# Kernel optimization log

Hardware: AMD Instinct MI355X
Metric: run time of the kernel (lower is better)

Reference implementation:

```python
import jax, jax.numpy as jnp
import numpy as np

EPS = 1e-06  # slot-attention renorm epsilon
LN_EPS = 1e-05  # torch LayerNorm default
NUM_ITERS = 3


def layernorm(x, w, b):
    m = jnp.mean(x, axis=-1, keepdims=True)
    v = jnp.mean((x - m) ** 2, axis=-1, keepdims=True)
    return (x - m) * jax.lax.rsqrt(v + LN_EPS) * w + b


def setup_inputs() -> dict:
    key = jax.random.key(0)
    ks = jax.random.split(key, 16)
    B, N, D = 32, 4096, 512
    S, NS, H = 128, 8, 256
    def lin(k, out_f, in_f):
        return jax.random.normal(k, (out_f, in_f), jnp.float32) * (1.0 / np.sqrt(in_f))
    return {
        "inputs": jax.random.normal(ks[0], (B, N, D), jnp.float32),
        "slots_init": jax.random.normal(ks[1], (B, NS, S), jnp.float32),
        "ln_in_w": jnp.ones((D,), jnp.float32), "ln_in_b": jnp.zeros((D,), jnp.float32),
        "ln_slot_w": jnp.ones((S,), jnp.float32), "ln_slot_b": jnp.zeros((S,), jnp.float32),
        "ln_mlp_w": jnp.ones((S,), jnp.float32), "ln_mlp_b": jnp.zeros((S,), jnp.float32),
        "Wq": lin(ks[2], S, S), "Wk": lin(ks[3], S, D), "Wv": lin(ks[4], S, D),
        "gru_Wih": lin(ks[5], 3 * S, S), "gru_Whh": lin(ks[6], 3 * S, S),
        "gru_bih": jnp.zeros((3 * S,), jnp.float32), "gru_bhh": jnp.zeros((3 * S,), jnp.float32),
        "mlp_W1": lin(ks[7], H, S), "mlp_b1": jnp.zeros((H,), jnp.float32),
        "mlp_W2": lin(ks[8], S, H), "mlp_b2": jnp.zeros((S,), jnp.float32),
        "slots_mu": jax.random.normal(ks[9], (1, 1, S), jnp.float32) * 0.1,
        "slots_log_sigma": jax.random.normal(ks[10], (1, 1, S), jnp.float32) * 0.1,
    }


def gru_cell(x, h, Wih, Whh, bih, bhh):
    # PyTorch GRUCell math. x, h: [BS, S]
    S = h.shape[-1]
    gi = x @ Wih.T + bih
    gh = h @ Whh.T + bhh
    i_r, i_z, i_n = gi[:, :S], gi[:, S:2 * S], gi[:, 2 * S:]
    h_r, h_z, h_n = gh[:, :S], gh[:, S:2 * S], gh[:, 2 * S:]
    r = jax.nn.sigmoid(i_r + h_r)
    z = jax.nn.sigmoid(i_z + h_z)
    n = jnp.tanh(i_n + r * h_n)
    return (1.0 - z) * n + z * h


def reference(inputs, slots_init, ln_in_w, ln_in_b, ln_slot_w, ln_slot_b, ln_mlp_w, ln_mlp_b,
              Wq, Wk, Wv, gru_Wih, gru_Whh, gru_bih, gru_bhh,
              mlp_W1, mlp_b1, mlp_W2, mlp_b2, slots_mu, slots_log_sigma):
    B, N, D = inputs.shape
    NS, S = slots_init.shape[1], slots_init.shape[2]
    x = layernorm(inputs, ln_in_w, ln_in_b)
    k = jnp.einsum('bnd,sd->bns', x, Wk)  # [B,N,S]
    v = jnp.einsum('bnd,sd->bns', x, Wv)
    slots = slots_mu + jnp.exp(slots_log_sigma) * slots_init  # [B,NS,S]
    scale = S ** (-0.5)
    for _ in range(NUM_ITERS):
        slots_prev = slots
        q = jnp.einsum('bmd,sd->bms', layernorm(slots, ln_slot_w, ln_slot_b), Wq)  # [B,NS,S]
        attn_logits = scale * jnp.einsum('bns,bms->bnm', k, q)  # [B,N,NS]
        attn = jax.nn.softmax(attn_logits, axis=-1) + EPS
        attn = attn / jnp.sum(attn, axis=1, keepdims=True)  # normalize over inputs
        updates = jnp.einsum('bnm,bns->bms', attn, v)  # [B,NS,S]
        h = gru_cell(updates.reshape(B * NS, S), slots_prev.reshape(B * NS, S),
                     gru_Wih, gru_Whh, gru_bih, gru_bhh).reshape(B, NS, S)
        mlp_out = jnp.maximum(layernorm(h, ln_mlp_w, ln_mlp_b) @ mlp_W1.T + mlp_b1, 0.0) @ mlp_W2.T + mlp_b2
        slots = h + mlp_out
    return slots
```

## Files before the change

### kernel.cpp

```cpp
#include <hip/hip_runtime.h>

typedef __bf16 v8bf __attribute__((ext_vector_type(8)));
typedef __bf16 v4bf __attribute__((ext_vector_type(4)));
typedef float  v4f  __attribute__((ext_vector_type(4)));
typedef unsigned short u16;

#define LN_EPS_F 1e-5f
#define ATTN_EPS 1e-6f

static constexpr int Bsz = 32;
static constexpr int Nn  = 4096;
static constexpr int Dd  = 512;
static constexpr int Ss  = 128;
static constexpr int NSs = 8;
static constexpr int Hh  = 256;
static constexpr int MROWS = Bsz * Nn;

__device__ __forceinline__ void load_lds16(const void* g, void* l) {
    __builtin_amdgcn_global_load_lds(
        (const __attribute__((address_space(1))) void*)g,
        (__attribute__((address_space(3))) void*)l, 16, 0, 0);
}

__global__ __launch_bounds__(256) void k_cast(const float* __restrict__ X,
                                              u16* __restrict__ Xb,
                                              float2* __restrict__ stats) {
    const int wid = threadIdx.x >> 6, lane = threadIdx.x & 63;
    const int row = blockIdx.x * 4 + wid;
    const float4* xp = reinterpret_cast<const float4*>(X + (size_t)row * Dd) + lane * 2;
    float4 a = xp[0];
    float4 b = xp[1];
    float s  = a.x + a.y + a.z + a.w + b.x + b.y + b.z + b.w;
    float s2 = a.x*a.x + a.y*a.y + a.z*a.z + a.w*a.w
             + b.x*b.x + b.y*b.y + b.z*b.z + b.w*b.w;
    v8bf o;
    o[0] = (__bf16)a.x; o[1] = (__bf16)a.y; o[2] = (__bf16)a.z; o[3] = (__bf16)a.w;
    o[4] = (__bf16)b.x; o[5] = (__bf16)b.y; o[6] = (__bf16)b.z; o[7] = (__bf16)b.w;
    *reinterpret_cast<v8bf*>(Xb + (size_t)row * Dd + lane * 8) = o;
#pragma unroll
    for (int off = 32; off > 0; off >>= 1) {
        s  += __shfl_xor(s, off);
        s2 += __shfl_xor(s2, off);
    }
    if (lane == 0) {
        float m = s * (1.0f / Dd);
        float v = s2 * (1.0f / Dd) - m * m;
        stats[row] = make_float2(m, rsqrtf(v + LN_EPS_F));
    }
}

__global__ __launch_bounds__(256) void k_prep(const float* __restrict__ Wk, const float* __restrict__ Wv,
                                              const float* __restrict__ ln_in_w, const float* __restrict__ ln_in_b,
                                              const float* __restrict__ slots_init, const float* __restrict__ mu,
                                              const float* __restrict__ lsig,
                                              u16* __restrict__ Wkvp, float* __restrict__ cb,
                                              float* __restrict__ Scol, float* __restrict__ slots) {
    const int bid = blockIdx.x;
    const int t = threadIdx.x;
    if (bid < 512) {
        int idx = bid * 256 + t;
        int n = idx >> 9, d = idx & 511;
        float w = (n < Ss) ? Wk[n * Dd + d] : Wv[(n - Ss) * Dd + d];
        w *= ln_in_w[d];
        __bf16 bv = (__bf16)w;
        Wkvp[idx] = __builtin_bit_cast(u16, bv);
    } else if (bid < 640) {
        int idx = (bid - 512) * 256 + t;
        int sidx = idx & (Ss - 1);
        slots[idx] = mu[sidx] + expf(lsig[sidx]) * slots_init[idx];
    } else {
        const int wid = t >> 6, lane = t & 63;
        const int rowbase = (bid - 640) * 32 + wid * 8;
        const int d0 = lane * 8;
        float4 lw0 = *reinterpret_cast<const float4*>(ln_in_w + d0);
        float4 lw1 = *reinterpret_cast<const float4*>(ln_in_w + d0 + 4);
        float4 lb0 = *reinterpret_cast<const float4*>(ln_in_b + d0);
        float4 lb1 = *reinterpret_cast<const float4*>(ln_in_b + d0 + 4);
        for (int rr = 0; rr < 8; ++rr) {
            int row = rowbase + rr;
            const float* wrow = (row < Ss) ? (Wk + (size_t)row * Dd)
                                           : (Wv + (size_t)(row - Ss) * Dd);
            float4 w0 = *reinterpret_cast<const float4*>(wrow + d0);
            float4 w1 = *reinterpret_cast<const float4*>(wrow + d0 + 4);
            float accb = lb0.x*w0.x + lb0.y*w0.y + lb0.z*w0.z + lb0.w*w0.w
                       + lb1.x*w1.x + lb1.y*w1.y + lb1.z*w1.z + lb1.w*w1.w;
            float accs = (float)(__bf16)(w0.x*lw0.x) + (float)(__bf16)(w0.y*lw0.y)
                       + (float)(__bf16)(w0.z*lw0.z) + (float)(__bf16)(w0.w*lw0.w)
                       + (float)(__bf16)(w1.x*lw1.x) + (float)(__bf16)(w1.y*lw1.y)
                       + (float)(__bf16)(w1.z*lw1.z) + (float)(__bf16)(w1.w*lw1.w);
#pragma unroll
            for (int off = 32; off > 0; off >>= 1) {
                accb += __shfl_xor(accb, off);
                accs += __shfl_xor(accs, off);
            }
            if (lane == 0) { cb[row] = accb; Scol[row] = accs; }
        }
    }
}

__global__ __launch_bounds__(512, 2) void k_kvgemm(const u16* __restrict__ Xb,
                                                   const float2* __restrict__ stats,
                                                   const u16* __restrict__ Wkvp,
                                                   const float* __restrict__ cb,
                                                   const float* __restrict__ Scol,
                                                   u16* __restrict__ kv) {
    __shared__ __bf16 As[2][256 * 64];
    __shared__ __bf16 Bsh[2][256 * 64];
    __shared__ float2 stats_sh[256];
    const int t    = threadIdx.x;
    const int lane = t & 63;
    const int w    = t >> 6;
    const int wr   = w >> 2;
    const int wc   = w & 3;
    const int lr   = lane & 15;
    const int g    = lane >> 4;
    const int r7   = lane & 7;
    const size_t m0 = (size_t)blockIdx.x * 256;

    const int rowoff = lane >> 3;
    const int swz8   = ((lane & 7) ^ rowoff) * 8;
    const u16* asrc = Xb   + (m0 + w * 32 + rowoff) * 512 + swz8;
    const u16* bsrc = Wkvp + (size_t)(w * 32 + rowoff) * 512 + swz8;

    if (t < 256) stats_sh[t] = stats[m0 + t];

    const v4f vzero = {0.f, 0.f, 0.f, 0.f};
    v4f acc[8][4];
#pragma unroll
    for (int i = 0; i < 8; ++i)
#pragma unroll
        for (int j = 0; j < 4; ++j) acc[i][j] = vzero;

#define STAGE(buf, kb)                                                          \
    {                                                                           \
        _Pragma("unroll")                                                       \
        for (int i = 0; i < 4; ++i) {                                           \
            load_lds16(asrc + (size_t)i * 8 * 512 + (kb) * 64,                  \
                       &As[buf][(w * 32 + i * 8) * 64]);                        \
            load_lds16(bsrc + (size_t)i * 8 * 512 + (kb) * 64,                  \
                       &Bsh[buf][(w * 32 + i * 8) * 64]);                       \
        }                                                                       \
    }

    STAGE(0, 0);
    asm volatile("s_waitcnt vmcnt(0) lgkmcnt(0)" ::: "memory");
    __builtin_amdgcn_s_barrier();

    int buf = 0;
#pragma unroll
    for (int kb = 0; kb < 8; ++kb) {
        if (kb < 7) STAGE(buf ^ 1, kb + 1);
#pragma unroll
        for (int ks = 0; ks < 2; ++ks) {
            const int co = ((ks * 4 + g) ^ r7) * 8;
            v8bf a[8], b[4];
#pragma unroll
            for (int mi = 0; mi < 8; ++mi)
                a[mi] = *reinterpret_cast<const v8bf*>(
                    &As[buf][(wr * 128 + mi * 16 + lr) * 64 + co]);
#pragma unroll
            for (int ni = 0; ni < 4; ++ni)
                b[ni] = *reinterpret_cast<const v8bf*>(
                    &Bsh[buf][(wc * 64 + ni * 16 + lr) * 64 + co]);
#pragma unroll
            for (int ni = 0; ni < 4; ++ni)
#pragma unroll
                for (int mi = 0; mi < 8; ++mi)
                    acc[mi][ni] = __builtin_amdgcn_mfma_f32_16x16x32_bf16(a[mi], b[ni], acc[mi][ni], 0, 0, 0);
        }
        asm volatile("s_waitcnt vmcnt(0)" ::: "memory");
        __builtin_amdgcn_s_barrier();
        buf ^= 1;
    }
#undef STAGE
    float Sn[4], cbv[4];
#pragma unroll
    for (int ni = 0; ni < 4; ++ni) {
        int col = wc * 64 + ni * 16 + lr;
        Sn[ni]  = Scol[col];
        cbv[ni] = cb[col];
    }
#pragma unroll
    for (int mi = 0; mi < 8; ++mi)
#pragma unroll
        for (int j = 0; j < 4; ++j) {
            int rl = wr * 128 + mi * 16 + g * 4 + j;
            float2 st = stats_sh[rl];
            size_t mg = m0 + rl;
#pragma unroll
            for (int ni = 0; ni < 4; ++ni) {
                int col = wc * 64 + ni * 16 + lr;
                float val = st.y * (acc[mi][ni][j] - st.x * Sn[ni]) + cbv[ni];
                __bf16 bv = (__bf16)val;
                kv[mg * 256 + col] = __builtin_bit_cast(u16, bv);
            }
        }
}

__global__ __launch_bounds__(128) void k_q(const float* __restrict__ slots,
                                           const float* __restrict__ lnw, const float* __restrict__ lnb,
                                           const float* __restrict__ Wq, float* __restrict__ q) {
    __shared__ float xs[128];
    __shared__ float red[4];
    const int t = threadIdx.x;
    const int bm = blockIdx.x;
    float x = slots[bm * 128 + t];
    float s = x, s2 = x * x;
#pragma unroll
    for (int off = 32; off > 0; off >>= 1) { s += __shfl_xor(s, off); s2 += __shfl_xor(s2, off); }
    const int wid = t >> 6, lane = t & 63;
    if (lane == 0) { red[wid * 2] = s; red[wid * 2 + 1] = s2; }
    __syncthreads();
    float S1 = red[0] + red[2], S2 = red[1] + red[3];
    float m = S1 * (1.f / 128.f);
    float rstd = rsqrtf(S2 * (1.f / 128.f) - m * m + LN_EPS_F);
    xs[t] = (x - m) * rstd * lnw[t] + lnb[t];
    __syncthreads();
    const float* wr = Wq + (size_t)t * 128;
    float acc = 0.f;
#pragma unroll 8
    for (int d = 0; d < 128; d += 4) {
        float4 w = *reinterpret_cast<const float4*>(wr + d);
        acc += w.x * xs[d] + w.y * xs[d + 1] + w.z * xs[d + 2] + w.w * xs[d + 3];
    }
    q[bm * 128 + t] = acc * 0.08838834764831845f;
}

__global__ __launch_bounds__(256) void k_attnupd(const u16* __restrict__ kv, const float* __restrict__ q,
                                                 float* __restrict__ upd_part, float* __restrict__ colsum_part) {
    __shared__ float qs[8 * 128];
    __shared__ float at[128][8];
    __shared__ __bf16 vt[128][128];
    __shared__ float colpart[4][8];
    const int b  = blockIdx.y;
    const int ch = blockIdx.x;
    const int t  = threadIdx.x;
    const int lane = t & 63, wv = t >> 6;
    *reinterpret_cast<float4*>(&qs[t * 4]) = *reinterpret_cast<const float4*>(&q[b * 1024 + t * 4]);
    __syncthreads();
    {
        const int rsub = lane >> 4;
        const int csub = (lane & 15) * 8;
#pragma unroll
        for (int p = 0; p < 8; ++p) {
            int row = wv * 32 + p * 4;
            const u16* src = kv + ((size_t)(b * Nn + ch * 128 + row + rsub)) * 256 + 128 + csub;
            load_lds16(src, &vt[row][0]);
        }
    }
    const int nl   = t >> 1;
    const int half = t & 1;
    const u16* krow = kv + ((size_t)(b * Nn + ch * 128 + nl)) * 256 + half * 64;
    float acc[8] = {0.f, 0.f, 0.f, 0.f, 0.f, 0.f, 0.f, 0.f};
#pragma unroll
    for (int c = 0; c < 8; ++c) {
        v8bf kvv = *reinterpret_cast<const v8bf*>(krow + c * 8);
        float kf[8];
#pragma unroll
        for (int j = 0; j < 8; ++j) kf[j] = (float)kvv[j];
#pragma unroll
        for (int m = 0; m < 8; ++m) {
            const float* qrow = &qs[m * 128 + half * 64 + c * 8];
            float aa = 0.f;
#pragma unroll
            for (int j = 0; j < 8; ++j) aa += kf[j] * qrow[j];
            acc[m] += aa;
        }
    }
#pragma unroll
    for (int m = 0; m < 8; ++m) acc[m] += __shfl_xor(acc[m], 1);
    float mx = acc[0];
#pragma unroll
    for (int m = 1; m < 8; ++m) mx = fmaxf(mx, acc[m]);
    float e[8]; float ssum = 0.f;
#pragma unroll
    for (int m = 0; m < 8; ++m) { e[m] = __expf(acc[m] - mx); ssum += e[m]; }
    float inv = 1.0f / ssum;
    float a8[8];
#pragma unroll
    for (int m = 0; m < 8; ++m) a8[m] = e[m] * inv + ATTN_EPS;
    *reinterpret_cast<float4*>(&at[nl][half * 4]) =
        make_float4(a8[half * 4], a8[half * 4 + 1], a8[half * 4 + 2], a8[half * 4 + 3]);
#pragma unroll
    for (int m = 0; m < 8; ++m) {
        float v = a8[m];
#pragma unroll
        for (int off = 32; off > 0; off >>= 1) v += __shfl_xor(v, off);
        if (lane == 0) colpart[wv][m] = v * 0.5f;
    }
    __syncthreads();
    const int m2 = t >> 5;
    const int s0 = (t & 31) * 4;
    float a0 = 0.f, a1 = 0.f, a2 = 0.f, a3 = 0.f;
#pragma unroll 4
    for (int n = 0; n < 128; ++n) {
        float a = at[n][m2];
        v4bf vvv = *reinterpret_cast<const v4bf*>(&vt[n][s0]);
        a0 += a * (float)vvv[0];
        a1 += a * (float)vvv[1];
        a2 += a * (float)vvv[2];
        a3 += a * (float)vvv[3];
    }
    *reinterpret_cast<float4*>(upd_part + ((size_t)(b * 32 + ch) * 8 + m2) * 128 + s0) =
        make_float4(a0, a1, a2, a3);
    if (t < 8)
        colsum_part[(b * 32 + ch) * 8 + t] =
            colpart[0][t] + colpart[1][t] + colpart[2][t] + colpart[3][t];
}

__global__ __launch_bounds__(256) void k_finishq(const float* __restrict__ upd_part,
                                                 const float* __restrict__ colsum_part,
                                                 const float* __restrict__ slots_in,
                                                 const float* __restrict__ Wih, const float* __restrict__ Whh,
                                                 const float* __restrict__ bih, const float* __restrict__ bhh,
                                                 const float* __restrict__ lnw, const float* __restrict__ lnb,
                                                 const float* __restrict__ W1, const float* __restrict__ b1,
                                                 const float* __restrict__ W2, const float* __restrict__ b2,
                                                 const float* __restrict__ lnsw, const float* __restrict__ lnsb,
                                                 const float* __restrict__ Wq,
                                                 float* __restrict__ slots_out, float* __restrict__ qout) {
    __shared__ float us[128], sp[128], hnorm[128], qsrc[128], act[256];
    __shared__ float upart[2][128];
    __shared__ float gpart[2][6][128];
    __shared__ float p2[2][128];
    __shared__ float qpart[2][128];
    __shared__ float red[4];
    __shared__ float csum_sh;
    const int t   = threadIdx.x;
    const int tid = t & 127, half = t >> 7;
    const int bm  = blockIdx.x;
    const int b = bm >> 3, m = bm & 7;
    if (t < 64) {
        float v = (t < 32) ? colsum_part[(b * 32 + t) * 8 + m] : 0.f;
#pragma unroll
        for (int off = 32; off > 0; off >>= 1) v += __shfl_xor(v, off);
        if (t == 0) csum_sh = v;
    }
    float u = 0.f;
#pragma unroll 4
    for (int chk = half * 16; chk < half * 16 + 16; ++chk)
        u += upd_part[((size_t)(b * 32 + chk) * 8 + m) * 128 + tid];
    upart[half][tid] = u;
    if (half == 0) sp[tid] = slots_in[bm * 128 + tid];
    __syncthreads();
    if (half == 0) us[tid] = (upart[0][tid] + upart[1][tid]) * (1.f / csum_sh);
    __syncthreads();
    {
        const int d0g = half * 64;
        float a_r = 0.f, a_z = 0.f, a_n = 0.f, b_r = 0.f, b_z = 0.f, b_n = 0.f;
        const float* Wr = Wih + (size_t)tid * 128 + d0g;
        const float* Wz = Wih + (size_t)(128 + tid) * 128 + d0g;
        const float* Wn = Wih + (size_t)(256 + tid) * 128 + d0g;
        const float* Vr = Whh + (size_t)tid * 128 + d0g;
        const float* Vz = Whh + (size_t)(128 + tid) * 128 + d0g;
        const float* Vn = Whh + (size_t)(256 + tid) * 128 + d0g;
#pragma unroll 4
        for (int d = 0; d < 64; d += 4) {
            float u0 = us[d0g + d], u1 = us[d0g + d + 1], u2 = us[d0g + d + 2], u3 = us[d0g + d + 3];
            float p0 = sp[d0g + d], p1 = sp[d0g + d + 1], p2_ = sp[d0g + d + 2], p3 = sp[d0g + d + 3];
            float4 w;
            w = *reinterpret_cast<const float4*>(Wr + d); a_r += w.x*u0 + w.y*u1 + w.z*u2 + w.w*u3;
            w = *reinterpret_cast<const float4*>(Wz + d); a_z += w.x*u0 + w.y*u1 + w.z*u2 + w.w*u3;
            w = *reinterpret_cast<const float4*>(Wn + d); a_n += w.x*u0 + w.y*u1 + w.z*u2 + w.w*u3;
            w = *reinterpret_cast<const float4*>(Vr + d); b_r += w.x*p0 + w.y*p1 + w.z*p2_ + w.w*p3;
            w = *reinterpret_cast<const float4*>(Vz + d); b_z += w.x*p0 + w.y*p1 + w.z*p2_ + w.w*p3;
            w = *reinterpret_cast<const float4*>(Vn + d); b_n += w.x*p0 + w.y*p1 + w.z*p2_ + w.w*p3;
        }
        gpart[half][0][tid] = a_r; gpart[half][1][tid] = a_z; gpart[half][2][tid] = a_n;
        gpart[half][3][tid] = b_r; gpart[half][4][tid] = b_z; gpart[half][5][tid] = b_n;
    }
    __syncthreads();
    float gir = bih[tid]       + gpart[0][0][tid] + gpart[1][0][tid];
    float giz = bih[128 + tid] + gpart[0][1][tid] + gpart[1][1][tid];
    float gin = bih[256 + tid] + gpart[0][2][tid] + gpart[1][2][tid];
    float ghr = bhh[tid]       + gpart[0][3][tid] + gpart[1][3][tid];
    float ghz = bhh[128 + tid] + gpart[0][4][tid] + gpart[1][4][tid];
    float ghn = bhh[256 + tid] + gpart[0][5][tid] + gpart[1][5][tid];
    float h0 = sp[tid];
    float r  = 1.f / (1.f + __expf(-(gir + ghr)));
    float z  = 1.f / (1.f + __expf(-(giz + ghz)));
    float nn = tanhf(gin + r * ghn);
    float h  = (1.f - z) * nn + z * h0;
    if (half == 0) {
        float s = h, s2 = h * h;
#pragma unroll
        for (int off = 32; off > 0; off >>= 1) { s += __shfl_xor(s, off); s2 += __shfl_xor(s2, off); }
        if ((t & 63) == 0) { red[(tid >> 6) * 2] = s; red[(tid >> 6) * 2 + 1] = s2; }
    }
    __syncthreads();
    {
        float S1 = red[0] + red[2], S2 = red[1] + red[3];
        float mean = S1 * (1.f / Ss);
        float rstd = rsqrtf(S2 * (1.f / Ss) - mean * mean + LN_EPS_F);
        if (half == 0) hnorm[tid] = (h - mean) * rstd * lnw[tid] + lnb[tid];
    }
    __syncthreads();
    {
        float a = b1[t];
        const float* w1r = W1 + (size_t)t * 128;
#pragma unroll 4
        for (int d = 0; d < 128; d += 4) {
            float4 w = *reinterpret_cast<const float4*>(w1r + d);
            a += w.x * hnorm[d] + w.y * hnorm[d + 1] + w.z * hnorm[d + 2] + w.w * hnorm[d + 3];
        }
        act[t] = fmaxf(a, 0.f);
    }
    __syncthreads();
    {
        float o = 0.f;
        const int j0 = half * 128;
        const float* w2r = W2 + (size_t)tid * 256 + j0;
#pragma unroll 4
        for (int j = 0; j < 128; j += 4) {
            float4 w = *reinterpret_cast<const float4*>(w2r + j);
            o += w.x * act[j0 + j] + w.y * act[j0 + j + 1] + w.z * act[j0 + j + 2] + w.w * act[j0 + j + 3];
        }
        p2[half][tid] = o;
    }
    __syncthreads();
    float snew = h + b2[tid] + p2[0][tid] + p2[1][tid];
    if (half == 0) slots_out[bm * 128 + tid] = snew;
    if (half == 0) {
        float s = snew, s2 = snew * snew;
#pragma unroll
        for (int off = 32; off > 0; off >>= 1) { s += __shfl_xor(s, off); s2 += __shfl_xor(s2, off); }
        if ((t & 63) == 0) { red[(tid >> 6) * 2] = s; red[(tid >> 6) * 2 + 1] = s2; }
    }
    __syncthreads();
    {
        float T1 = red[0] + red[2], T2 = red[1] + red[3];
        float m2 = T1 * (1.f / Ss);
        float rstd2 = rsqrtf(T2 * (1.f / Ss) - m2 * m2 + LN_EPS_F);
        if (half == 0) qsrc[tid] = (snew - m2) * rstd2 * lnsw[tid] + lnsb[tid];
    }
    __syncthreads();
    {
        float qa = 0.f;
        const int d0g = half * 64;
        const float* wr = Wq + (size_t)tid * 128 + d0g;
#pragma unroll 4
        for (int d = 0; d < 64; d += 4) {
            float4 w = *reinterpret_cast<const float4*>(wr + d);
            qa += w.x * qsrc[d0g + d] + w.y * qsrc[d0g + d + 1] + w.z * qsrc[d0g + d + 2] + w.w * qsrc[d0g + d + 3];
        }
        qpart[half][tid] = qa;
    }
    __syncthreads();
    if (half == 0)
        qout[bm * 128 + tid] = (qpart[0][tid] + qpart[1][tid]) * 0.08838834764831845f;
}

extern "C" void kernel_launch(void* const* d_in, const int* in_sizes, int n_in,
                              void* d_out, int out_size, void* d_ws, size_t ws_size,
                              hipStream_t stream) {
    const float* X          = (const float*)d_in[0];
    const float* slots_init = (const float*)d_in[1];
    const float* ln_in_w    = (const float*)d_in[2];
    const float* ln_in_b    = (const float*)d_in[3];
    const float* ln_slot_w  = (const float*)d_in[4];
    const float* ln_slot_b  = (const float*)d_in[5];
    const float* ln_mlp_w   = (const float*)d_in[6];
    const float* ln_mlp_b   = (const float*)d_in[7];
    const float* Wq         = (const float*)d_in[8];
    const float* Wk         = (const float*)d_in[9];
    const float* Wv         = (const float*)d_in[10];
    const float* gWih       = (const float*)d_in[11];
    const float* gWhh       = (const float*)d_in[12];
    const float* gbih       = (const float*)d_in[13];
    const float* gbhh       = (const float*)d_in[14];
    const float* W1         = (const float*)d_in[15];
    const float* b1         = (const float*)d_in[16];
    const float* W2         = (const float*)d_in[17];
    const float* b2         = (const float*)d_in[18];
    const float* mu         = (const float*)d_in[19];
    const float* lsig       = (const float*)d_in[20];

    char* p = (char*)d_ws;
    u16*    Wkvp        = (u16*)p;    p += (size_t)256 * 512 * sizeof(u16);
    float*  cb          = (float*)p;  p += 256 * sizeof(float);
    float*  Scol        = (float*)p;  p += 256 * sizeof(float);
    float*  slots       = (float*)p;  p += 32 * 8 * 128 * sizeof(float);
    float*  qbuf        = (float*)p;  p += 32 * 8 * 128 * sizeof(float);
    float*  colsum_part = (float*)p;  p += 32 * 32 * 8 * sizeof(float);
    float*  upd_part    = (float*)p;  p += (size_t)32 * 32 * 8 * 128 * sizeof(float);
    u16*    kv          = (u16*)p;    p += (size_t)MROWS * 256 * sizeof(u16);
    u16*    Xb          = (u16*)p;    p += (size_t)MROWS * Dd * sizeof(u16);
    float2* stats       = (float2*)p; p += (size_t)MROWS * sizeof(float2);

    k_cast<<<MROWS / 4, 256, 0, stream>>>(X, Xb, stats);
    k_prep<<<648, 256, 0, stream>>>(Wk, Wv, ln_in_w, ln_in_b, slots_init, mu, lsig,
                                    Wkvp, cb, Scol, slots);
    k_kvgemm<<<MROWS / 256, 512, 0, stream>>>(Xb, stats, Wkvp, cb, Scol, kv);
    k_q<<<256, 128, 0, stream>>>(slots, ln_slot_w, ln_slot_b, Wq, qbuf);

    for (int it = 0; it < 3; ++it) {
        k_attnupd<<<dim3(32, 32), 256, 0, stream>>>(kv, qbuf, upd_part, colsum_part);
        k_finishq<<<256, 256, 0, stream>>>(upd_part, colsum_part, slots,
                                           gWih, gWhh, gbih, gbhh,
                                           ln_mlp_w, ln_mlp_b, W1, b1, W2, b2,
                                           ln_slot_w, ln_slot_b, Wq,
                                           (it == 2) ? (float*)d_out : slots, qbuf);
    }
}
```

Baseline: 317.6 us.

## Fold Wk/Wv projections into slot side, attend directly over normalized inputs

```diff
diff --git a/kernel.cpp b/kernel.cpp
--- a/kernel.cpp
+++ b/kernel.cpp
@@ -49,152 +49,37 @@
     }
 }
 
-__global__ __launch_bounds__(256) void k_prep(const float* __restrict__ Wk, const float* __restrict__ Wv,
-                                              const float* __restrict__ ln_in_w, const float* __restrict__ ln_in_b,
-                                              const float* __restrict__ slots_init, const float* __restrict__ mu,
+__global__ __launch_bounds__(256) void k_prep(const float* __restrict__ Wv,
+                                              const float* __restrict__ ln_in_b,
+                                              const float* __restrict__ slots_init,
+                                              const float* __restrict__ mu,
                                               const float* __restrict__ lsig,
-                                              u16* __restrict__ Wkvp, float* __restrict__ cb,
-                                              float* __restrict__ Scol, float* __restrict__ slots) {
+                                              float* __restrict__ cbv0,
+                                              float* __restrict__ slots) {
     const int bid = blockIdx.x;
     const int t = threadIdx.x;
-    if (bid < 512) {
+    if (bid < 128) {
         int idx = bid * 256 + t;
-        int n = idx >> 9, d = idx & 511;
-        float w = (n < Ss) ? Wk[n * Dd + d] : Wv[(n - Ss) * Dd + d];
-        w *= ln_in_w[d];
-        __bf16 bv = (__bf16)w;
-        Wkvp[idx] = __builtin_bit_cast(u16, bv);
-    } else if (bid < 640) {
-        int idx = (bid - 512) * 256 + t;
         int sidx = idx & (Ss - 1);
         slots[idx] = mu[sidx] + expf(lsig[sidx]) * slots_init[idx];
     } else {
         const int wid = t >> 6, lane = t & 63;
-        const int rowbase = (bid - 640) * 32 + wid * 8;
+        const int rowbase = (bid - 128) * 32 + wid * 8;
         const int d0 = lane * 8;
-        float4 lw0 = *reinterpret_cast<const float4*>(ln_in_w + d0);
-        float4 lw1 = *reinterpret_cast<const float4*>(ln_in_w + d0 + 4);
         float4 lb0 = *reinterpret_cast<const float4*>(ln_in_b + d0);
         float4 lb1 = *reinterpret_cast<const float4*>(ln_in_b + d0 + 4);
         for (int rr = 0; rr < 8; ++rr) {
             int row = rowbase + rr;
-            const float* wrow = (row < Ss) ? (Wk + (size_t)row * Dd)
-                                           : (Wv + (size_t)(row - Ss) * Dd);
+            const float* wrow = Wv + (size_t)row * Dd;
             float4 w0 = *reinterpret_cast<const float4*>(wrow + d0);
             float4 w1 = *reinterpret_cast<const float4*>(wrow + d0 + 4);
             float accb = lb0.x*w0.x + lb0.y*w0.y + lb0.z*w0.z + lb0.w*w0.w
                        + lb1.x*w1.x + lb1.y*w1.y + lb1.z*w1.z + lb1.w*w1.w;
-            float accs = (float)(__bf16)(w0.x*lw0.x) + (float)(__bf16)(w0.y*lw0.y)
-                       + (float)(__bf16)(w0.z*lw0.z) + (float)(__bf16)(w0.w*lw0.w)
-                       + (float)(__bf16)(w1.x*lw1.x) + (float)(__bf16)(w1.y*lw1.y)
-                       + (float)(__bf16)(w1.z*lw1.z) + (float)(__bf16)(w1.w*lw1.w);
-#pragma unroll
-            for (int off = 32; off > 0; off >>= 1) {
-                accb += __shfl_xor(accb, off);
-                accs += __shfl_xor(accs, off);
-            }
-            if (lane == 0) { cb[row] = accb; Scol[row] = accs; }
-        }
-    }
-}
-
-__global__ __launch_bounds__(512, 2) void k_kvgemm(const u16* __restrict__ Xb,
-                                                   const float2* __restrict__ stats,
-                                                   const u16* __restrict__ Wkvp,
-                                                   const float* __restrict__ cb,
-                                                   const float* __restrict__ Scol,
-                                                   u16* __restrict__ kv) {
-    __shared__ __bf16 As[2][256 * 64];
-    __shared__ __bf16 Bsh[2][256 * 64];
-    __shared__ float2 stats_sh[256];
-    const int t    = threadIdx.x;
-    const int lane = t & 63;
-    const int w    = t >> 6;
-    const int wr   = w >> 2;
-    const int wc   = w & 3;
-    const int lr   = lane & 15;
-    const int g    = lane >> 4;
-    const int r7   = lane & 7;
-    const size_t m0 = (size_t)blockIdx.x * 256;
-
-    const int rowoff = lane >> 3;
-    const int swz8   = ((lane & 7) ^ rowoff) * 8;
-    const u16* asrc = Xb   + (m0 + w * 32 + rowoff) * 512 + swz8;
-    const u16* bsrc = Wkvp + (size_t)(w * 32 + rowoff) * 512 + swz8;
-
-    if (t < 256) stats_sh[t] = stats[m0 + t];
-
-    const v4f vzero = {0.f, 0.f, 0.f, 0.f};
-    v4f acc[8][4];
-#pragma unroll
-    for (int i = 0; i < 8; ++i)
-#pragma unroll
-        for (int j = 0; j < 4; ++j) acc[i][j] = vzero;
-
-#define STAGE(buf, kb)                                                          \
-    {                                                                           \
-        _Pragma("unroll")                                                       \
-        for (int i = 0; i < 4; ++i) {                                           \
-            load_lds16(asrc + (size_t)i * 8 * 512 + (kb) * 64,                  \
-                       &As[buf][(w * 32 + i * 8) * 64]);                        \
-            load_lds16(bsrc + (size_t)i * 8 * 512 + (kb) * 64,                  \
-                       &Bsh[buf][(w * 32 + i * 8) * 64]);                       \
-        }                                                                       \
-    }
-
-    STAGE(0, 0);
-    asm volatile("s_waitcnt vmcnt(0) lgkmcnt(0)" ::: "memory");
-    __builtin_amdgcn_s_barrier();
-
-    int buf = 0;
-#pragma unroll
-    for (int kb = 0; kb < 8; ++kb) {
-        if (kb < 7) STAGE(buf ^ 1, kb + 1);
-#pragma unroll
-        for (int ks = 0; ks < 2; ++ks) {
-            const int co = ((ks * 4 + g) ^ r7) * 8;
-            v8bf a[8], b[4];
-#pragma unroll
-            for (int mi = 0; mi < 8; ++mi)
-                a[mi] = *reinterpret_cast<const v8bf*>(
-                    &As[buf][(wr * 128 + mi * 16 + lr) * 64 + co]);
-#pragma unroll
-            for (int ni = 0; ni < 4; ++ni)
-                b[ni] = *reinterpret_cast<const v8bf*>(
-                    &Bsh[buf][(wc * 64 + ni * 16 + lr) * 64 + co]);
-#pragma unroll
-            for (int ni = 0; ni < 4; ++ni)
-#pragma unroll
-                for (int mi = 0; mi < 8; ++mi)
-                    acc[mi][ni] = __builtin_amdgcn_mfma_f32_16x16x32_bf16(a[mi], b[ni], acc[mi][ni], 0, 0, 0);
-        }
-        asm volatile("s_waitcnt vmcnt(0)" ::: "memory");
-        __builtin_amdgcn_s_barrier();
-        buf ^= 1;
-    }
-#undef STAGE
-    float Sn[4], cbv[4];
-#pragma unroll
-    for (int ni = 0; ni < 4; ++ni) {
-        int col = wc * 64 + ni * 16 + lr;
-        Sn[ni]  = Scol[col];
-        cbv[ni] = cb[col];
-    }
-#pragma unroll
-    for (int mi = 0; mi < 8; ++mi)
-#pragma unroll
-        for (int j = 0; j < 4; ++j) {
-            int rl = wr * 128 + mi * 16 + g * 4 + j;
-            float2 st = stats_sh[rl];
-            size_t mg = m0 + rl;
-#pragma unroll
-            for (int ni = 0; ni < 4; ++ni) {
-                int col = wc * 64 + ni * 16 + lr;
-                float val = st.y * (acc[mi][ni][j] - st.x * Sn[ni]) + cbv[ni];
-                __bf16 bv = (__bf16)val;
-                kv[mg * 256 + col] = __builtin_bit_cast(u16, bv);
-            }
-        }
+#pragma unroll
+            for (int off = 32; off > 0; off >>= 1) accb += __shfl_xor(accb, off);
+            if (lane == 0) cbv0[row] = accb;
+        }
+    }
 }
 
 __global__ __launch_bounds__(128) void k_q(const float* __restrict__ slots,
@@ -226,91 +111,186 @@
     q[bm * 128 + t] = acc * 0.08838834764831845f;
 }
 
-__global__ __launch_bounds__(256) void k_attnupd(const u16* __restrict__ kv, const float* __restrict__ q,
-                                                 float* __restrict__ upd_part, float* __restrict__ colsum_part) {
-    __shared__ float qs[8 * 128];
-    __shared__ float at[128][8];
-    __shared__ __bf16 vt[128][128];
-    __shared__ float colpart[4][8];
+__global__ __launch_bounds__(256) void k_wlgen(const float* __restrict__ qbuf,
+                                               const float* __restrict__ Wk,
+                                               const float* __restrict__ lnw,
+                                               const float* __restrict__ lnb,
+                                               u16* __restrict__ wl,
+                                               float* __restrict__ Sw,
+                                               float* __restrict__ cw) {
+    const int m = blockIdx.x, b = blockIdx.y;
+    const int t = threadIdx.x;
+    u16* outrow = wl + ((size_t)b * 16 + m) * 512;
+    if (m >= 8) {
+        outrow[t] = 0; outrow[t + 256] = 0;
+        if (t == 0) { Sw[b * 16 + m] = 0.f; cw[b * 16 + m] = 0.f; }
+        return;
+    }
+    __shared__ float qsh[128];
+    __shared__ float rs[4], rc[4];
+    if (t < 128) qsh[t] = qbuf[(b * 8 + m) * 128 + t];
+    __syncthreads();
+    float acc0 = 0.f, acc1 = 0.f;
+#pragma unroll 4
+    for (int s = 0; s < 128; ++s) {
+        float qv = qsh[s];
+        acc0 += qv * Wk[(size_t)s * 512 + t];
+        acc1 += qv * Wk[(size_t)s * 512 + t + 256];
+    }
+    float wl0 = lnw[t] * acc0, wl1 = lnw[t + 256] * acc1;
+    __bf16 b0 = (__bf16)wl0, b1 = (__bf16)wl1;
+    outrow[t] = __builtin_bit_cast(u16, b0);
+    outrow[t + 256] = __builtin_bit_cast(u16, b1);
+    float swp = (float)b0 + (float)b1;
+    float cwp = lnb[t] * acc0 + lnb[t + 256] * acc1;
+#pragma unroll
+    for (int off = 32; off > 0; off >>= 1) { swp += __shfl_xor(swp, off); cwp += __shfl_xor(cwp, off); }
+    const int lane = t & 63, wv = t >> 6;
+    if (lane == 0) { rs[wv] = swp; rc[wv] = cwp; }
+    __syncthreads();
+    if (t == 0) {
+        Sw[b * 16 + m] = rs[0] + rs[1] + rs[2] + rs[3];
+        cw[b * 16 + m] = rc[0] + rc[1] + rc[2] + rc[3];
+    }
+}
+
+__global__ __launch_bounds__(256, 1) void k_attnz(const u16* __restrict__ Xb,
+                                                  const float2* __restrict__ stats,
+                                                  const u16* __restrict__ wl,
+                                                  const float* __restrict__ Sw,
+                                                  const float* __restrict__ cw,
+                                                  float* __restrict__ z_part,
+                                                  float* __restrict__ A_part,
+                                                  float* __restrict__ cm_part) {
+    __shared__ __bf16 xs[2][64 * 512];
+    __shared__ __bf16 wls[16 * 512];
+    __shared__ float at[64][8];
+    __shared__ float redA[4][8], redC[4][8];
     const int b  = blockIdx.y;
     const int ch = blockIdx.x;
     const int t  = threadIdx.x;
-    const int lane = t & 63, wv = t >> 6;
-    *reinterpret_cast<float4*>(&qs[t * 4]) = *reinterpret_cast<const float4*>(&q[b * 1024 + t * 4]);
-    __syncthreads();
-    {
-        const int rsub = lane >> 4;
-        const int csub = (lane & 15) * 8;
-#pragma unroll
-        for (int p = 0; p < 8; ++p) {
-            int row = wv * 32 + p * 4;
-            const u16* src = kv + ((size_t)(b * Nn + ch * 128 + row + rsub)) * 256 + 128 + csub;
-            load_lds16(src, &vt[row][0]);
-        }
-    }
-    const int nl   = t >> 1;
-    const int half = t & 1;
-    const u16* krow = kv + ((size_t)(b * Nn + ch * 128 + nl)) * 256 + half * 64;
-    float acc[8] = {0.f, 0.f, 0.f, 0.f, 0.f, 0.f, 0.f, 0.f};
-#pragma unroll
-    for (int c = 0; c < 8; ++c) {
-        v8bf kvv = *reinterpret_cast<const v8bf*>(krow + c * 8);
-        float kf[8];
-#pragma unroll
-        for (int j = 0; j < 8; ++j) kf[j] = (float)kvv[j];
-#pragma unroll
-        for (int m = 0; m < 8; ++m) {
-            const float* qrow = &qs[m * 128 + half * 64 + c * 8];
-            float aa = 0.f;
-#pragma unroll
-            for (int j = 0; j < 8; ++j) aa += kf[j] * qrow[j];
-            acc[m] += aa;
-        }
-    }
-#pragma unroll
-    for (int m = 0; m < 8; ++m) acc[m] += __shfl_xor(acc[m], 1);
-    float mx = acc[0];
-#pragma unroll
-    for (int m = 1; m < 8; ++m) mx = fmaxf(mx, acc[m]);
-    float e[8]; float ssum = 0.f;
-#pragma unroll
-    for (int m = 0; m < 8; ++m) { e[m] = __expf(acc[m] - mx); ssum += e[m]; }
-    float inv = 1.0f / ssum;
-    float a8[8];
-#pragma unroll
-    for (int m = 0; m < 8; ++m) a8[m] = e[m] * inv + ATTN_EPS;
-    *reinterpret_cast<float4*>(&at[nl][half * 4]) =
-        make_float4(a8[half * 4], a8[half * 4 + 1], a8[half * 4 + 2], a8[half * 4 + 3]);
-#pragma unroll
-    for (int m = 0; m < 8; ++m) {
-        float v = a8[m];
-#pragma unroll
-        for (int off = 32; off > 0; off >>= 1) v += __shfl_xor(v, off);
-        if (lane == 0) colpart[wv][m] = v * 0.5f;
-    }
-    __syncthreads();
-    const int m2 = t >> 5;
-    const int s0 = (t & 31) * 4;
-    float a0 = 0.f, a1 = 0.f, a2 = 0.f, a3 = 0.f;
-#pragma unroll 4
-    for (int n = 0; n < 128; ++n) {
-        float a = at[n][m2];
-        v4bf vvv = *reinterpret_cast<const v4bf*>(&vt[n][s0]);
-        a0 += a * (float)vvv[0];
-        a1 += a * (float)vvv[1];
-        a2 += a * (float)vvv[2];
-        a3 += a * (float)vvv[3];
-    }
-    *reinterpret_cast<float4*>(upd_part + ((size_t)(b * 32 + ch) * 8 + m2) * 128 + s0) =
-        make_float4(a0, a1, a2, a3);
-    if (t < 8)
-        colsum_part[(b * 32 + ch) * 8 + t] =
-            colpart[0][t] + colpart[1][t] + colpart[2][t] + colpart[3][t];
-}
-
-__global__ __launch_bounds__(256) void k_finishq(const float* __restrict__ upd_part,
-                                                 const float* __restrict__ colsum_part,
+    const int lane = t & 63, w = t >> 6;
+    const int lr = lane & 15, g = lane >> 4;
+    const size_t nbase = (size_t)b * Nn + ch * 256;
+
+    {
+        int row = t >> 4;
+#pragma unroll
+        for (int c = 0; c < 4; ++c) {
+            int s = (t & 15) * 4 + c;
+            uint4 v = *reinterpret_cast<const uint4*>(wl + ((size_t)b * 16 + row) * 512 + s * 8);
+            *reinterpret_cast<uint4*>(&wls[row * 512 + (s ^ (row & 7)) * 8]) = v;
+        }
+    }
+    const float Swm = Sw[b * 16 + lr];
+    const float cwm = cw[b * 16 + lr];
+
+    const int zm = t >> 5;
+    const int ds = t & 31;
+    float z[16];
+#pragma unroll
+    for (int i = 0; i < 16; ++i) z[i] = 0.f;
+    float A_acc = 0.f, C_acc = 0.f;
+
+#define STAGE(buf, sub)                                                         \
+    {                                                                           \
+        _Pragma("unroll")                                                       \
+        for (int i = 0; i < 16; ++i) {                                          \
+            int r = w * 16 + i;                                                 \
+            load_lds16(Xb + (nbase + (sub) * 64 + r) * 512 + (lane ^ (r & 7)) * 8, \
+                       &xs[buf][r * 512]);                                      \
+        }                                                                       \
+    }
+
+    STAGE(0, 0);
+    asm volatile("s_waitcnt vmcnt(0)" ::: "memory");
+    __syncthreads();
+
+    int cur = 0;
+    const v4f vzero = {0.f, 0.f, 0.f, 0.f};
+#pragma unroll 1
+    for (int sub = 0; sub < 4; ++sub) {
+        if (sub < 3) STAGE(cur ^ 1, sub + 1);
+        v4f D = vzero;
+        {
+            const __bf16* arow = &xs[cur][(w * 16 + lr) * 512];
+            const __bf16* brow = &wls[lr * 512];
+            const int sw = lr & 7;
+#pragma unroll
+            for (int kk = 0; kk < 16; ++kk) {
+                int sl = ((kk * 4 + g) ^ sw) * 8;
+                v8bf a  = *reinterpret_cast<const v8bf*>(arow + sl);
+                v8bf bb = *reinterpret_cast<const v8bf*>(brow + sl);
+                D = __builtin_amdgcn_mfma_f32_16x16x32_bf16(a, bb, D, 0, 0, 0);
+            }
+        }
+        float2 st[4];
+#pragma unroll
+        for (int j = 0; j < 4; ++j)
+            st[j] = stats[nbase + sub * 64 + w * 16 + g * 4 + j];
+#pragma unroll
+        for (int j = 0; j < 4; ++j) {
+            float lg = (lr < 8) ? (st[j].y * (D[j] - st[j].x * Swm) + cwm) : -1e30f;
+            float mx = lg;
+            mx = fmaxf(mx, __shfl_xor(mx, 1));
+            mx = fmaxf(mx, __shfl_xor(mx, 2));
+            mx = fmaxf(mx, __shfl_xor(mx, 4));
+            float e = __expf(lg - mx);
+            float sme = e;
+            sme += __shfl_xor(sme, 1);
+            sme += __shfl_xor(sme, 2);
+            sme += __shfl_xor(sme, 4);
+            float a = e / sme + ATTN_EPS;
+            if (lr < 8) {
+                at[w * 16 + g * 4 + j][lr] = a * st[j].y;
+                A_acc += a;
+                C_acc += a * st[j].y * st[j].x;
+            }
+        }
+        __syncthreads();
+        {
+            const __bf16* xcur = &xs[cur][0];
+#pragma unroll 4
+            for (int n = 0; n < 64; ++n) {
+                float av = at[n][zm];
+                int r7 = n & 7;
+                v8bf x0 = *reinterpret_cast<const v8bf*>(xcur + n * 512 + ((2 * ds)     ^ r7) * 8);
+                v8bf x1 = *reinterpret_cast<const v8bf*>(xcur + n * 512 + ((2 * ds + 1) ^ r7) * 8);
+#pragma unroll
+                for (int i = 0; i < 8; ++i) z[i]     += av * (float)x0[i];
+#pragma unroll
+                for (int i = 0; i < 8; ++i) z[8 + i] += av * (float)x1[i];
+            }
+        }
+        asm volatile("s_waitcnt vmcnt(0)" ::: "memory");
+        __syncthreads();
+        cur ^= 1;
+    }
+#undef STAGE
+    {
+        float* zp = z_part + (((size_t)(b * 16 + ch) * 8 + zm) * 512 + ds * 16);
+#pragma unroll
+        for (int c = 0; c < 4; ++c)
+            *reinterpret_cast<float4*>(zp + c * 4) =
+                make_float4(z[c * 4], z[c * 4 + 1], z[c * 4 + 2], z[c * 4 + 3]);
+    }
+    A_acc += __shfl_xor(A_acc, 16); A_acc += __shfl_xor(A_acc, 32);
+    C_acc += __shfl_xor(C_acc, 16); C_acc += __shfl_xor(C_acc, 32);
+    if (g == 0 && lr < 8) { redA[w][lr] = A_acc; redC[w][lr] = C_acc; }
+    __syncthreads();
+    if (t < 8) {
+        A_part[(b * 16 + ch) * 8 + t]  = redA[0][t] + redA[1][t] + redA[2][t] + redA[3][t];
+        cm_part[(b * 16 + ch) * 8 + t] = redC[0][t] + redC[1][t] + redC[2][t] + redC[3][t];
+    }
+}
+
+__global__ __launch_bounds__(256) void k_finishq(const float* __restrict__ z_part,
+                                                 const float* __restrict__ A_part,
+                                                 const float* __restrict__ cm_part,
                                                  const float* __restrict__ slots_in,
+                                                 const float* __restrict__ Wv,
+                                                 const float* __restrict__ cbv0,
+                                                 const float* __restrict__ lnw_in,
                                                  const float* __restrict__ Wih, const float* __restrict__ Whh,
                                                  const float* __restrict__ bih, const float* __restrict__ bhh,
                                                  const float* __restrict__ lnw, const float* __restrict__ lnb,
@@ -319,31 +299,50 @@
                                                  const float* __restrict__ lnsw, const float* __restrict__ lnsb,
                                                  const float* __restrict__ Wq,
                                                  float* __restrict__ slots_out, float* __restrict__ qout) {
+    __shared__ float zsh[512];
     __shared__ float us[128], sp[128], hnorm[128], qsrc[128], act[256];
     __shared__ float upart[2][128];
     __shared__ float gpart[2][6][128];
     __shared__ float p2[2][128];
     __shared__ float qpart[2][128];
     __shared__ float red[4];
-    __shared__ float csum_sh;
+    __shared__ float A_sh, cm_sh;
     const int t   = threadIdx.x;
     const int tid = t & 127, half = t >> 7;
     const int bm  = blockIdx.x;
     const int b = bm >> 3, m = bm & 7;
-    if (t < 64) {
-        float v = (t < 32) ? colsum_part[(b * 32 + t) * 8 + m] : 0.f;
-#pragma unroll
-        for (int off = 32; off > 0; off >>= 1) v += __shfl_xor(v, off);
-        if (t == 0) csum_sh = v;
-    }
-    float u = 0.f;
-#pragma unroll 4
-    for (int chk = half * 16; chk < half * 16 + 16; ++chk)
-        u += upd_part[((size_t)(b * 32 + chk) * 8 + m) * 128 + tid];
-    upart[half][tid] = u;
+    if (t < 16) {
+        float av = A_part[(b * 16 + t) * 8 + m];
+        float cv = cm_part[(b * 16 + t) * 8 + m];
+#pragma unroll
+        for (int off = 8; off > 0; off >>= 1) { av += __shfl_xor(av, off); cv += __shfl_xor(cv, off); }
+        if (t == 0) { A_sh = av; cm_sh = cv; }
+    }
     if (half == 0) sp[tid] = slots_in[bm * 128 + tid];
-    __syncthreads();
-    if (half == 0) us[tid] = (upart[0][tid] + upart[1][tid]) * (1.f / csum_sh);
+    float z0 = 0.f, z1 = 0.f;
+#pragma unroll 4
+    for (int ch = 0; ch < 16; ++ch) {
+        const float* zp = z_part + ((size_t)(b * 16 + ch) * 8 + m) * 512;
+        z0 += zp[t];
+        z1 += zp[t + 256];
+    }
+    __syncthreads();
+    zsh[t]       = (z0 - cm_sh) * lnw_in[t];
+    zsh[t + 256] = (z1 - cm_sh) * lnw_in[t + 256];
+    __syncthreads();
+    {
+        float acc = 0.f;
+        const float* wvp = Wv + (size_t)tid * 512 + half * 256;
+        const float* zz  = zsh + half * 256;
+#pragma unroll 4
+        for (int d = 0; d < 256; d += 4) {
+            float4 w = *reinterpret_cast<const float4*>(wvp + d);
+            acc += w.x * zz[d] + w.y * zz[d + 1] + w.z * zz[d + 2] + w.w * zz[d + 3];
+        }
+        upart[half][tid] = acc;
+    }
+    __syncthreads();
+    if (half == 0) us[tid] = (upart[0][tid] + upart[1][tid]) * (1.f / A_sh) + cbv0[tid];
     __syncthreads();
     {
         const int d0g = half * 64;
@@ -476,26 +475,29 @@
     const float* lsig       = (const float*)d_in[20];
 
     char* p = (char*)d_ws;
-    u16*    Wkvp        = (u16*)p;    p += (size_t)256 * 512 * sizeof(u16);
-    float*  cb          = (float*)p;  p += 256 * sizeof(float);
-    float*  Scol        = (float*)p;  p += 256 * sizeof(float);
-    float*  slots       = (float*)p;  p += 32 * 8 * 128 * sizeof(float);
-    float*  qbuf        = (float*)p;  p += 32 * 8 * 128 * sizeof(float);
-    float*  colsum_part = (float*)p;  p += 32 * 32 * 8 * sizeof(float);
-    float*  upd_part    = (float*)p;  p += (size_t)32 * 32 * 8 * 128 * sizeof(float);
-    u16*    kv          = (u16*)p;    p += (size_t)MROWS * 256 * sizeof(u16);
-    u16*    Xb          = (u16*)p;    p += (size_t)MROWS * Dd * sizeof(u16);
-    float2* stats       = (float2*)p; p += (size_t)MROWS * sizeof(float2);
+    float*  cbv0    = (float*)p;  p += 128 * sizeof(float);
+    float*  slots   = (float*)p;  p += 32 * 8 * 128 * sizeof(float);
+    float*  qbuf    = (float*)p;  p += 32 * 8 * 128 * sizeof(float);
+    u16*    wlbuf   = (u16*)p;    p += (size_t)32 * 16 * 512 * sizeof(u16);
+    float*  Swb     = (float*)p;  p += 32 * 16 * sizeof(float);
+    float*  cwb     = (float*)p;  p += 32 * 16 * sizeof(float);
+    float*  A_part  = (float*)p;  p += 32 * 16 * 8 * sizeof(float);
+    float*  cm_part = (float*)p;  p += 32 * 16 * 8 * sizeof(float);
+    float*  z_part  = (float*)p;  p += (size_t)32 * 16 * 8 * 512 * sizeof(float);
+    u16*    Xb      = (u16*)p;    p += (size_t)MROWS * Dd * sizeof(u16);
+    float2* stats   = (float2*)p; p += (size_t)MROWS * sizeof(float2);
 
     k_cast<<<MROWS / 4, 256, 0, stream>>>(X, Xb, stats);
-    k_prep<<<648, 256, 0, stream>>>(Wk, Wv, ln_in_w, ln_in_b, slots_init, mu, lsig,
-                                    Wkvp, cb, Scol, slots);
-    k_kvgemm<<<MROWS / 256, 512, 0, stream>>>(Xb, stats, Wkvp, cb, Scol, kv);
+    k_prep<<<132, 256, 0, stream>>>(Wv, ln_in_b, slots_init, mu, lsig, cbv0, slots);
     k_q<<<256, 128, 0, stream>>>(slots, ln_slot_w, ln_slot_b, Wq, qbuf);
 
     for (int it = 0; it < 3; ++it) {
-        k_attnupd<<<dim3(32, 32), 256, 0, stream>>>(kv, qbuf, upd_part, colsum_part);
-        k_finishq<<<256, 256, 0, stream>>>(upd_part, colsum_part, slots,
+        k_wlgen<<<dim3(16, 32), 256, 0, stream>>>(qbuf, Wk, ln_in_w, ln_in_b,
+                                                  wlbuf, Swb, cwb);
+        k_attnz<<<dim3(16, 32), 256, 0, stream>>>(Xb, stats, wlbuf, Swb, cwb,
+                                                  z_part, A_part, cm_part);
+        k_finishq<<<256, 256, 0, stream>>>(z_part, A_part, cm_part, slots,
+                                           Wv, cbv0, ln_in_w,
                                            gWih, gWhh, gbih, gbhh,
                                            ln_mlp_w, ln_mlp_b, W1, b1, W2, b2,
                                            ln_slot_w, ln_slot_b, Wq,
```

After: 440.3 us. 1.39x slower.

## Fuse fp32-to-bf16 cast and LayerNorm stats into the KV GEMM prologue

Applied to the files above, without the earlier changes.

```diff
diff --git a/kernel.cpp b/kernel.cpp
--- a/kernel.cpp
+++ b/kernel.cpp
@@ -20,33 +20,6 @@
     __builtin_amdgcn_global_load_lds(
         (const __attribute__((address_space(1))) void*)g,
         (__attribute__((address_space(3))) void*)l, 16, 0, 0);
-}
-
-__global__ __launch_bounds__(256) void k_cast(const float* __restrict__ X,
-                                              u16* __restrict__ Xb,
-                                              float2* __restrict__ stats) {
-    const int wid = threadIdx.x >> 6, lane = threadIdx.x & 63;
-    const int row = blockIdx.x * 4 + wid;
-    const float4* xp = reinterpret_cast<const float4*>(X + (size_t)row * Dd) + lane * 2;
-    float4 a = xp[0];
-    float4 b = xp[1];
-    float s  = a.x + a.y + a.z + a.w + b.x + b.y + b.z + b.w;
-    float s2 = a.x*a.x + a.y*a.y + a.z*a.z + a.w*a.w
-             + b.x*b.x + b.y*b.y + b.z*b.z + b.w*b.w;
-    v8bf o;
-    o[0] = (__bf16)a.x; o[1] = (__bf16)a.y; o[2] = (__bf16)a.z; o[3] = (__bf16)a.w;
-    o[4] = (__bf16)b.x; o[5] = (__bf16)b.y; o[6] = (__bf16)b.z; o[7] = (__bf16)b.w;
-    *reinterpret_cast<v8bf*>(Xb + (size_t)row * Dd + lane * 8) = o;
-#pragma unroll
-    for (int off = 32; off > 0; off >>= 1) {
-        s  += __shfl_xor(s, off);
-        s2 += __shfl_xor(s2, off);
-    }
-    if (lane == 0) {
-        float m = s * (1.0f / Dd);
-        float v = s2 * (1.0f / Dd) - m * m;
-        stats[row] = make_float2(m, rsqrtf(v + LN_EPS_F));
-    }
 }
 
 __global__ __launch_bounds__(256) void k_prep(const float* __restrict__ Wk, const float* __restrict__ Wv,
@@ -98,12 +71,11 @@
     }
 }
 
-__global__ __launch_bounds__(512, 2) void k_kvgemm(const u16* __restrict__ Xb,
-                                                   const float2* __restrict__ stats,
-                                                   const u16* __restrict__ Wkvp,
-                                                   const float* __restrict__ cb,
-                                                   const float* __restrict__ Scol,
-                                                   u16* __restrict__ kv) {
+__global__ __launch_bounds__(512) void k_kvgemm(const float* __restrict__ X,
+                                                const u16* __restrict__ Wkvp,
+                                                const float* __restrict__ cb,
+                                                const float* __restrict__ Scol,
+                                                u16* __restrict__ kv) {
     __shared__ __bf16 As[2][256 * 64];
     __shared__ __bf16 Bsh[2][256 * 64];
     __shared__ float2 stats_sh[256];
@@ -117,12 +89,15 @@
     const int r7   = lane & 7;
     const size_t m0 = (size_t)blockIdx.x * 256;
 
+    const int ar   = t >> 1;
+    const int agr  = (t & 1) * 4;
+    const int ar7  = ar & 7;
+    const float* xrow = X + (m0 + ar) * Dd + agr * 8;
+    __bf16* adst = &As[0][ar * 64];
+
     const int rowoff = lane >> 3;
     const int swz8   = ((lane & 7) ^ rowoff) * 8;
-    const u16* asrc = Xb   + (m0 + w * 32 + rowoff) * 512 + swz8;
-    const u16* bsrc = Wkvp + (size_t)(w * 32 + rowoff) * 512 + swz8;
-
-    if (t < 256) stats_sh[t] = stats[m0 + t];
+    const u16* bsrc = Wkvp + (size_t)(w * 32 + rowoff) * Dd + swz8;
 
     const v4f vzero = {0.f, 0.f, 0.f, 0.f};
     v4f acc[8][4];
@@ -131,25 +106,49 @@
 #pragma unroll
         for (int j = 0; j < 4; ++j) acc[i][j] = vzero;
 
-#define STAGE(buf, kb)                                                          \
+    float s1 = 0.f, s2 = 0.f;
+
+#define STAGE_B(buf, kb)                                                        \
     {                                                                           \
         _Pragma("unroll")                                                       \
-        for (int i = 0; i < 4; ++i) {                                           \
-            load_lds16(asrc + (size_t)i * 8 * 512 + (kb) * 64,                  \
-                       &As[buf][(w * 32 + i * 8) * 64]);                        \
-            load_lds16(bsrc + (size_t)i * 8 * 512 + (kb) * 64,                  \
+        for (int i = 0; i < 4; ++i)                                             \
+            load_lds16(bsrc + (size_t)i * 8 * Dd + (kb) * 64,                   \
                        &Bsh[buf][(w * 32 + i * 8) * 64]);                       \
-        }                                                                       \
-    }
-
-    STAGE(0, 0);
-    asm volatile("s_waitcnt vmcnt(0) lgkmcnt(0)" ::: "memory");
-    __builtin_amdgcn_s_barrier();
-
-    int buf = 0;
+    }
+
+    float4 a_pre[8];
+#pragma unroll
+    for (int j = 0; j < 8; ++j)
+        a_pre[j] = *reinterpret_cast<const float4*>(xrow + j * 4);
+    STAGE_B(0, 0);
+
 #pragma unroll
     for (int kb = 0; kb < 8; ++kb) {
-        if (kb < 7) STAGE(buf ^ 1, kb + 1);
+        const int buf = kb & 1;
+        __bf16* ad = adst + buf * (256 * 64);
+#pragma unroll
+        for (int g4 = 0; g4 < 4; ++g4) {
+            float4 lo = a_pre[g4 * 2];
+            float4 hi = a_pre[g4 * 2 + 1];
+            s1 += lo.x + lo.y + lo.z + lo.w + hi.x + hi.y + hi.z + hi.w;
+            s2 += lo.x*lo.x + lo.y*lo.y + lo.z*lo.z + lo.w*lo.w
+                + hi.x*hi.x + hi.y*hi.y + hi.z*hi.z + hi.w*hi.w;
+            v8bf o;
+            o[0] = (__bf16)lo.x; o[1] = (__bf16)lo.y; o[2] = (__bf16)lo.z; o[3] = (__bf16)lo.w;
+            o[4] = (__bf16)hi.x; o[5] = (__bf16)hi.y; o[6] = (__bf16)hi.z; o[7] = (__bf16)hi.w;
+            *reinterpret_cast<v8bf*>(ad + ((agr + g4) ^ ar7) * 8) = o;
+        }
+        if (kb < 7) {
+#pragma unroll
+            for (int j = 0; j < 8; ++j)
+                a_pre[j] = *reinterpret_cast<const float4*>(xrow + (kb + 1) * 64 + j * 4);
+        }
+        if (kb < 7) STAGE_B(buf ^ 1, kb + 1);
+        if (kb < 7)
+            asm volatile("s_waitcnt vmcnt(12) lgkmcnt(0)" ::: "memory");
+        else
+            asm volatile("s_waitcnt vmcnt(0) lgkmcnt(0)" ::: "memory");
+        __builtin_amdgcn_s_barrier();
 #pragma unroll
         for (int ks = 0; ks < 2; ++ks) {
             const int co = ((ks * 4 + g) ^ r7) * 8;
@@ -168,11 +167,17 @@
                 for (int mi = 0; mi < 8; ++mi)
                     acc[mi][ni] = __builtin_amdgcn_mfma_f32_16x16x32_bf16(a[mi], b[ni], acc[mi][ni], 0, 0, 0);
         }
-        asm volatile("s_waitcnt vmcnt(0)" ::: "memory");
         __builtin_amdgcn_s_barrier();
-        buf ^= 1;
-    }
-#undef STAGE
+    }
+#undef STAGE_B
+    s1 += __shfl_xor(s1, 1);
+    s2 += __shfl_xor(s2, 1);
+    if ((t & 1) == 0) {
+        float m = s1 * (1.f / Dd);
+        float v = s2 * (1.f / Dd) - m * m;
+        stats_sh[ar] = make_float2(m, rsqrtf(v + LN_EPS_F));
+    }
+    __syncthreads();
     float Sn[4], cbv[4];
 #pragma unroll
     for (int ni = 0; ni < 4; ++ni) {
@@ -484,13 +489,10 @@
     float*  colsum_part = (float*)p;  p += 32 * 32 * 8 * sizeof(float);
     float*  upd_part    = (float*)p;  p += (size_t)32 * 32 * 8 * 128 * sizeof(float);
     u16*    kv          = (u16*)p;    p += (size_t)MROWS * 256 * sizeof(u16);
-    u16*    Xb          = (u16*)p;    p += (size_t)MROWS * Dd * sizeof(u16);
-    float2* stats       = (float2*)p; p += (size_t)MROWS * sizeof(float2);
-
-    k_cast<<<MROWS / 4, 256, 0, stream>>>(X, Xb, stats);
+
     k_prep<<<648, 256, 0, stream>>>(Wk, Wv, ln_in_w, ln_in_b, slots_init, mu, lsig,
                                     Wkvp, cb, Scol, slots);
-    k_kvgemm<<<MROWS / 256, 512, 0, stream>>>(Xb, stats, Wkvp, cb, Scol, kv);
+    k_kvgemm<<<MROWS / 256, 512, 0, stream>>>(X, Wkvp, cb, Scol, kv);
     k_q<<<256, 128, 0, stream>>>(slots, ln_slot_w, ln_slot_b, Wq, qbuf);
 
     for (int it = 0; it < 3; ++it) {
```

Measured after the change: 414.6 us. 1.31x slower.
